# Kernel tuning notes

Hardware: AMD Instinct MI355X
Metric: run time of the kernel (lower is better)

## Reference

```python
import jax, jax.numpy as jnp
import numpy as np

VOCAB = 100000
HIDDEN = 512
BATCH = 4096
TOTAL_TOKENS = 819200
BN_EPS = 1e-5


def setup_inputs() -> dict:
    key = jax.random.key(0)
    k_tok, k_seg, k_t, k_emb, k_wh, k_bh, k_wo, k_bo = jax.random.split(key, 8)
    tokens = jax.random.randint(k_tok, (TOTAL_TOKENS,), 0, VOCAB, dtype=jnp.int64 if jax.config.jax_enable_x64 else jnp.int32)
    segment_ids = jnp.sort(jax.random.randint(k_seg, (TOTAL_TOKENS,), 0, BATCH))
    t = jax.random.uniform(k_t, (BATCH,), dtype=jnp.float32)
    emb = jax.random.normal(k_emb, (VOCAB, HIDDEN), dtype=jnp.float32)
    bound = 1.0 / np.sqrt(HIDDEN)
    W_h = jax.random.uniform(k_wh, (HIDDEN, HIDDEN), minval=-bound, maxval=bound, dtype=jnp.float32)
    b_h = jax.random.uniform(k_bh, (HIDDEN,), minval=-bound, maxval=bound, dtype=jnp.float32)
    gamma = jnp.ones((HIDDEN,), jnp.float32)
    beta = jnp.zeros((HIDDEN,), jnp.float32)
    W_o = jax.random.uniform(k_wo, (HIDDEN,), minval=-bound, maxval=bound, dtype=jnp.float32)
    b_o = jax.random.uniform(k_bo, (), minval=-bound, maxval=bound, dtype=jnp.float32)
    return {"tokens": tokens, "segment_ids": segment_ids, "t": t, "emb": emb,
            "W_h": W_h, "b_h": b_h, "gamma": gamma, "beta": beta, "W_o": W_o, "b_o": b_o}


def reference(tokens, segment_ids, t, emb, W_h, b_h, gamma, beta, W_o, b_o):
    # Ragged bag-of-words: gather embeddings and mean-pool per segment (per review)
    tok_emb = emb[tokens]                                            # [T, H]
    sums = jax.ops.segment_sum(tok_emb, segment_ids, num_segments=BATCH)   # [B, H]
    counts = jax.ops.segment_sum(jnp.ones((tokens.shape[0],), emb.dtype),
                                 segment_ids, num_segments=BATCH)    # [B]
    pooled = sums / jnp.maximum(counts, 1.0)[:, None]                # [B, H]
    # fc_hidden -> BatchNorm1d (training mode, batch stats, biased var) -> ReLU
    h = pooled @ W_h + b_h
    mu = jnp.mean(h, axis=0)
    var = jnp.mean((h - mu) ** 2, axis=0)
    h = gamma * (h - mu) * jax.lax.rsqrt(var + BN_EPS) + beta
    h = jax.nn.relu(h)
    # dropout is identity at eval; fc_output -> logits
    logits = h @ W_o + b_o                                           # [B]
    # BCEWithLogitsLoss (mean): softplus(x) - t*x
    loss = jnp.mean(jax.nn.softplus(logits) - t * logits)
    return (loss, logits)
```

## Files before the change

kernel.cpp:

```cpp
#include <hip/hip_runtime.h>
#include <hip/hip_bf16.h>

#define BATCH 4096
#define HIDDEN 512
#define BN_EPS 1e-5f
#define STAGE_CAP 1024

typedef unsigned int u32;
typedef unsigned short u16;
typedef unsigned char u8;
typedef float f32x4 __attribute__((ext_vector_type(4)));
typedef __bf16 bf16x8 __attribute__((ext_vector_type(8)));

__device__ __forceinline__ float bf2f(u32 lo) { return __uint_as_float(lo << 16); }
__device__ __forceinline__ u32 f2bf(float f) {
    u32 u = __float_as_uint(f);
    return (u + 0x7FFFu + ((u >> 16) & 1u)) >> 16;
}

__device__ __forceinline__ int detect_bf16(const u32* __restrict__ emb_w) {
    u32 v = emb_w[(size_t)(threadIdx.x & 63) * 400009u + 17u];
    float a = fabsf(bf2f(v & 0xffffu));
    bool bf_like = (a > 0.0009765625f) && (a < 16.0f);
    unsigned long long m = __ballot(bf_like);
    return __popcll(m) >= 48;
}

__global__ __launch_bounds__(256) void k_convert(const void* __restrict__ emb,
                                                 u8* __restrict__ tab,
                                                 float* __restrict__ scales,
                                                 const void* __restrict__ W,
                                                 u16* __restrict__ Wt,
                                                 float* __restrict__ zero_base,
                                                 int vocab) {
    const int nrb = (vocab + 3) >> 2;
    if (blockIdx.x == (u32)(nrb + 64)) {
        for (int i = threadIdx.x; i < 2 * HIDDEN + 2; i += 256) zero_base[i] = 0.f;
        return;
    }
    const int bf = detect_bf16((const u32*)emb);
    if (blockIdx.x >= (u32)nrb) {
        __shared__ u16 tile[64][66];
        const int b2 = blockIdx.x - nrb;
        const int k0 = (b2 >> 3) * 64, n0 = (b2 & 7) * 64;
        const int c = threadIdx.x & 63, r4 = threadIdx.x >> 6;
#pragma unroll
        for (int i = 0; i < 16; ++i) {
            const int k = k0 + r4 + i * 4;
            u16 w;
            if (bf) w = ((const u16*)W)[(size_t)k * HIDDEN + n0 + c];
            else    w = (u16)f2bf(((const float*)W)[(size_t)k * HIDDEN + n0 + c]);
            tile[k - k0][c] = w;
        }
        __syncthreads();
#pragma unroll
        for (int i = 0; i < 16; ++i) {
            const int n = n0 + r4 + i * 4;
            Wt[(size_t)n * HIDDEN + k0 + c] = tile[c][n - n0];
        }
        return;
    }

    const int wv = threadIdx.x >> 6, lane = threadIdx.x & 63;
    const int row = blockIdx.x * 4 + wv;
    if (row >= vocab) return;

    float v[8];
    if (bf) {
        uint4 u = *(const uint4*)((const u16*)emb + (size_t)row * HIDDEN + lane * 8);
        v[0] = bf2f(u.x & 0xffffu); v[1] = bf2f(u.x >> 16);
        v[2] = bf2f(u.y & 0xffffu); v[3] = bf2f(u.y >> 16);
        v[4] = bf2f(u.z & 0xffffu); v[5] = bf2f(u.z >> 16);
        v[6] = bf2f(u.w & 0xffffu); v[7] = bf2f(u.w >> 16);
    } else {
        const f32x4* p = (const f32x4*)((const float*)emb + (size_t)row * HIDDEN + lane * 8);
        f32x4 a = __builtin_nontemporal_load(p);
        f32x4 b = __builtin_nontemporal_load(p + 1);
        v[0] = a.x; v[1] = a.y; v[2] = a.z; v[3] = a.w;
        v[4] = b.x; v[5] = b.y; v[6] = b.z; v[7] = b.w;
    }
    float m = 0.f;
#pragma unroll
    for (int k = 0; k < 8; ++k) m = fmaxf(m, fabsf(v[k]));
#pragma unroll
    for (int o = 32; o > 0; o >>= 1) m = fmaxf(m, __shfl_xor(m, o));
    const float s   = m * (1.0f / 127.0f);
    const float inv = (m > 0.f) ? (127.0f / m) : 0.f;
    int q[8];
#pragma unroll
    for (int k = 0; k < 8; ++k) q[k] = (int)rintf(v[k] * inv);
    uint2 o;
    o.x = (q[0] & 255) | ((q[1] & 255) << 8) | ((q[2] & 255) << 16) | ((u32)(q[3] & 255) << 24);
    o.y = (q[4] & 255) | ((q[5] & 255) << 8) | ((q[6] & 255) << 16) | ((u32)(q[7] & 255) << 24);
    *(uint2*)(tab + (size_t)row * HIDDEN + lane * 8) = o;
    if (lane == 0) scales[row] = s;
}

__global__ __launch_bounds__(256) void k_pool(const int* __restrict__ tokens,
                                              const int* __restrict__ seg,
                                              const void* __restrict__ emb,
                                              const u8* __restrict__ tab,
                                              const float* __restrict__ scales,
                                              int use_table,
                                              u32* __restrict__ pooled_bf, int T) {
    const int bf = detect_bf16((const u32*)emb);
    const int b = blockIdx.x;
    int lo = 0, hi = T;
    while (lo < hi) { int m = (lo + hi) >> 1; if (seg[m] < b) lo = m + 1; else hi = m; }
    const int start = lo;
    hi = T;
    while (lo < hi) { int m = (lo + hi) >> 1; if (seg[m] < b + 1) lo = m + 1; else hi = m; }
    const int end = lo;
    const int cnt = end - start;

    const int wv = threadIdx.x >> 6;
    const int lane = threadIdx.x & 63;
    const int chunk = (cnt + 3) >> 2;
    const int ts = start + wv * chunk;
    const int te = min(ts + chunk, end);

    float acc[8] = {0.f,0.f,0.f,0.f,0.f,0.f,0.f,0.f};

    __shared__ int   stok[STAGE_CAP];
    __shared__ float ssc[STAGE_CAP];

#define DECQ(v_, s_) \
    acc[0] = fmaf(s_, (float)(int)(signed char)( v_.x        & 255u), acc[0]); \
    acc[1] = fmaf(s_, (float)(int)(signed char)((v_.x >>  8) & 255u), acc[1]); \
    acc[2] = fmaf(s_, (float)(int)(signed char)((v_.x >> 16) & 255u), acc[2]); \
    acc[3] = fmaf(s_, (float)(int)(signed char)( v_.x >> 24        ), acc[3]); \
    acc[4] = fmaf(s_, (float)(int)(signed char)( v_.y        & 255u), acc[4]); \
    acc[5] = fmaf(s_, (float)(int)(signed char)((v_.y >>  8) & 255u), acc[5]); \
    acc[6] = fmaf(s_, (float)(int)(signed char)((v_.y >> 16) & 255u), acc[6]); \
    acc[7] = fmaf(s_, (float)(int)(signed char)( v_.y >> 24        ), acc[7]);

    if (use_table && cnt <= STAGE_CAP) {
        for (int i = threadIdx.x; i < cnt; i += 256) {
            const int tk = tokens[start + i];
            stok[i] = tk;
            ssc[i]  = scales[tk];
        }
        __syncthreads();
        int t = ts;
        for (; t + 4 <= te; t += 4) {
            const int i = t - start;
            const int tk0 = stok[i],     tk1 = stok[i + 1];
            const int tk2 = stok[i + 2], tk3 = stok[i + 3];
            const float s0 = ssc[i],     s1 = ssc[i + 1];
            const float s2 = ssc[i + 2], s3 = ssc[i + 3];
            uint2 v0 = *(const uint2*)(tab + (size_t)tk0 * HIDDEN + lane * 8);
            uint2 v1 = *(const uint2*)(tab + (size_t)tk1 * HIDDEN + lane * 8);
            uint2 v2 = *(const uint2*)(tab + (size_t)tk2 * HIDDEN + lane * 8);
            uint2 v3 = *(const uint2*)(tab + (size_t)tk3 * HIDDEN + lane * 8);
            DECQ(v0, s0); DECQ(v1, s1); DECQ(v2, s2); DECQ(v3, s3);
        }
        for (; t < te; ++t) {
            const int i = t - start;
            const int tk = stok[i];
            const float s = ssc[i];
            uint2 v = *(const uint2*)(tab + (size_t)tk * HIDDEN + lane * 8);
            DECQ(v, s);
        }
    } else if (use_table) {
        int t = ts;
        for (; t + 4 <= te; t += 4) {
            const int tk0 = tokens[t],     tk1 = tokens[t + 1];
            const int tk2 = tokens[t + 2], tk3 = tokens[t + 3];
            const float s0 = scales[tk0], s1 = scales[tk1];
            const float s2 = scales[tk2], s3 = scales[tk3];
            uint2 v0 = *(const uint2*)(tab + (size_t)tk0 * HIDDEN + lane * 8);
            uint2 v1 = *(const uint2*)(tab + (size_t)tk1 * HIDDEN + lane * 8);
            uint2 v2 = *(const uint2*)(tab + (size_t)tk2 * HIDDEN + lane * 8);
            uint2 v3 = *(const uint2*)(tab + (size_t)tk3 * HIDDEN + lane * 8);
            DECQ(v0, s0); DECQ(v1, s1); DECQ(v2, s2); DECQ(v3, s3);
        }
        for (; t < te; ++t) {
            const int tk = tokens[t];
            const float s = scales[tk];
            uint2 v = *(const uint2*)(tab + (size_t)tk * HIDDEN + lane * 8);
            DECQ(v, s);
        }
    } else if (bf) {
        const u16* src = (const u16*)emb;
        for (int t = ts; t < te; ++t) {
            uint4 v = *(const uint4*)(src + (size_t)tokens[t] * HIDDEN + lane * 8);
            acc[0] += bf2f(v.x & 0xffffu); acc[1] += bf2f(v.x >> 16);
            acc[2] += bf2f(v.y & 0xffffu); acc[3] += bf2f(v.y >> 16);
            acc[4] += bf2f(v.z & 0xffffu); acc[5] += bf2f(v.z >> 16);
            acc[6] += bf2f(v.w & 0xffffu); acc[7] += bf2f(v.w >> 16);
        }
    } else {
        const float* e = (const float*)emb;
        for (int t = ts; t < te; ++t) {
            const float* p = e + (size_t)tokens[t] * HIDDEN + lane * 8;
            float4 a = *(const float4*)p, b2_ = *(const float4*)(p + 4);
            acc[0] += a.x; acc[1] += a.y; acc[2] += a.z; acc[3] += a.w;
            acc[4] += b2_.x; acc[5] += b2_.y; acc[6] += b2_.z; acc[7] += b2_.w;
        }
    }
#undef DECQ

    __shared__ float red[4][8][64];
    if (wv > 0) {
#pragma unroll
        for (int k = 0; k < 8; ++k) red[wv][k][lane] = acc[k];
    }
    __syncthreads();
    if (wv == 0) {
#pragma unroll
        for (int k = 0; k < 8; ++k)
            acc[k] += red[1][k][lane] + red[2][k][lane] + red[3][k][lane];
        const float inv = (cnt > 0) ? (1.0f / (float)cnt) : 1.0f;
        uint4 o;
        o.x = f2bf(acc[0] * inv) | (f2bf(acc[1] * inv) << 16);
        o.y = f2bf(acc[2] * inv) | (f2bf(acc[3] * inv) << 16);
        o.z = f2bf(acc[4] * inv) | (f2bf(acc[5] * inv) << 16);
        o.w = f2bf(acc[6] * inv) | (f2bf(acc[7] * inv) << 16);
        *(uint4*)(pooled_bf + (size_t)b * (HIDDEN / 2) + lane * 4) = o;
    }
}

__global__ __launch_bounds__(256) void k_gemm(const u32* __restrict__ pooled_bf,
                                              const void* __restrict__ W,
                                              const u16* __restrict__ Wt,
                                              const void* __restrict__ bias,
                                              const u32* __restrict__ embw,
                                              int use_wt,
                                              float* __restrict__ h,
                                              float* __restrict__ sums,
                                              float* __restrict__ sumsq) {
    __shared__ float ws_s[4][4][16], ws_q[4][4][16];
    const int bf = detect_bf16(embw);
    const int tid  = threadIdx.x;
    const int wv   = tid >> 6;
    const int lane = tid & 63;
    const int l15  = lane & 15;
    const int hi   = lane >> 4;
    const int rb   = (blockIdx.x >> 3) * 64;
    const int nb   = (blockIdx.x & 7) * 64;
    const int mrow = rb + wv * 16 + l15;

    f32x4 acc[4] = {};

    for (int k0 = 0; k0 < HIDDEN; k0 += 32) {
        const int kb = k0 + hi * 8;
        uint4 av = *(const uint4*)(pooled_bf + (size_t)mrow * (HIDDEN / 2) + (kb >> 1));
        bf16x8 afrag = __builtin_bit_cast(bf16x8, av);
#pragma unroll
        for (int j = 0; j < 4; ++j) {
            const int n = nb + j * 16 + l15;
            bf16x8 bfrag;
            if (use_wt) {
                uint4 bv = *(const uint4*)(Wt + (size_t)n * HIDDEN + kb);
                bfrag = __builtin_bit_cast(bf16x8, bv);
            } else {
                u16 bw[8];
                if (bf) {
                    const u16* Wb = (const u16*)W;
#pragma unroll
                    for (int i = 0; i < 8; ++i) bw[i] = Wb[(size_t)(kb + i) * HIDDEN + n];
                } else {
                    const float* Wf = (const float*)W;
#pragma unroll
                    for (int i = 0; i < 8; ++i) bw[i] = (u16)f2bf(Wf[(size_t)(kb + i) * HIDDEN + n]);
                }
                uint4 bv;
                bv.x = bw[0] | ((u32)bw[1] << 16);
                bv.y = bw[2] | ((u32)bw[3] << 16);
                bv.z = bw[4] | ((u32)bw[5] << 16);
                bv.w = bw[6] | ((u32)bw[7] << 16);
                bfrag = __builtin_bit_cast(bf16x8, bv);
            }
            acc[j] = __builtin_amdgcn_mfma_f32_16x16x32_bf16(afrag, bfrag, acc[j], 0, 0, 0);
        }
    }

#pragma unroll
    for (int j = 0; j < 4; ++j) {
        const int n = nb + j * 16 + l15;
        const float bvn = bf ? bf2f(((const u16*)bias)[n]) : ((const float*)bias)[n];
        float s = 0.f, q = 0.f;
#pragma unroll
        for (int r = 0; r < 4; ++r) {
            const int row = rb + wv * 16 + hi * 4 + r;
            const float v = acc[j][r] + bvn;
            h[(size_t)row * HIDDEN + n] = v;
            s += v;
            q = fmaf(v, v, q);
        }
        s += __shfl_xor(s, 16); s += __shfl_xor(s, 32);
        q += __shfl_xor(q, 16); q += __shfl_xor(q, 32);
        if (lane < 16) { ws_s[wv][j][l15] = s; ws_q[wv][j][l15] = q; }
    }
    __syncthreads();
    if (tid < 64) {
        const int j2 = tid >> 4, c = tid & 15;
        float ts = ws_s[0][j2][c] + ws_s[1][j2][c] + ws_s[2][j2][c] + ws_s[3][j2][c];
        float tq = ws_q[0][j2][c] + ws_q[1][j2][c] + ws_q[2][j2][c] + ws_q[3][j2][c];
        atomicAdd(&sums[nb + j2 * 16 + c],  ts);
        atomicAdd(&sumsq[nb + j2 * 16 + c], tq);
    }
}

__global__ __launch_bounds__(256) void k_out(const float* __restrict__ h,
                                             const float* __restrict__ sums,
                                             const float* __restrict__ sumsq,
                                             const void* __restrict__ gamma,
                                             const void* __restrict__ beta,
                                             const void* __restrict__ W_o,
                                             const void* __restrict__ b_o,
                                             const void* __restrict__ tvec,
                                             const u32* __restrict__ embw,
                                             void* __restrict__ out,
                                             float* __restrict__ loss_acc,
                                             u32* __restrict__ counter) {
    const int bf = detect_bf16(embw);
    const int lane = threadIdx.x & 63;
    const int wave = threadIdx.x >> 6;
    const int row  = blockIdx.x * 4 + wave;
    const float invN = 1.0f / (float)BATCH;
    const int c0 = lane * 8;

    float g[8], bt[8], wo[8];
    if (bf) {
        uint4 gu = *(const uint4*)((const u32*)gamma + lane * 4);
        uint4 bu = *(const uint4*)((const u32*)beta  + lane * 4);
        uint4 wu = *(const uint4*)((const u32*)W_o   + lane * 4);
        g[0]=bf2f(gu.x&0xffffu); g[1]=bf2f(gu.x>>16); g[2]=bf2f(gu.y&0xffffu); g[3]=bf2f(gu.y>>16);
        g[4]=bf2f(gu.z&0xffffu); g[5]=bf2f(gu.z>>16); g[6]=bf2f(gu.w&0xffffu); g[7]=bf2f(gu.w>>16);
        bt[0]=bf2f(bu.x&0xffffu); bt[1]=bf2f(bu.x>>16); bt[2]=bf2f(bu.y&0xffffu); bt[3]=bf2f(bu.y>>16);
        bt[4]=bf2f(bu.z&0xffffu); bt[5]=bf2f(bu.z>>16); bt[6]=bf2f(bu.w&0xffffu); bt[7]=bf2f(bu.w>>16);
        wo[0]=bf2f(wu.x&0xffffu); wo[1]=bf2f(wu.x>>16); wo[2]=bf2f(wu.y&0xffffu); wo[3]=bf2f(wu.y>>16);
        wo[4]=bf2f(wu.z&0xffffu); wo[5]=bf2f(wu.z>>16); wo[6]=bf2f(wu.w&0xffffu); wo[7]=bf2f(wu.w>>16);
    } else {
        float4 a, b2;
        a = *(const float4*)((const float*)gamma + c0); b2 = *(const float4*)((const float*)gamma + c0 + 4);
        g[0]=a.x; g[1]=a.y; g[2]=a.z; g[3]=a.w; g[4]=b2.x; g[5]=b2.y; g[6]=b2.z; g[7]=b2.w;
        a = *(const float4*)((const float*)beta + c0);  b2 = *(const float4*)((const float*)beta + c0 + 4);
        bt[0]=a.x; bt[1]=a.y; bt[2]=a.z; bt[3]=a.w; bt[4]=b2.x; bt[5]=b2.y; bt[6]=b2.z; bt[7]=b2.w;
        a = *(const float4*)((const float*)W_o + c0);   b2 = *(const float4*)((const float*)W_o + c0 + 4);
        wo[0]=a.x; wo[1]=a.y; wo[2]=a.z; wo[3]=a.w; wo[4]=b2.x; wo[5]=b2.y; wo[6]=b2.z; wo[7]=b2.w;
    }

    float hv[8], sm[8], sq[8];
    {
        const float* hp = h + (size_t)row * HIDDEN + c0;
        float4 a = *(const float4*)hp, b2 = *(const float4*)(hp + 4);
        hv[0]=a.x; hv[1]=a.y; hv[2]=a.z; hv[3]=a.w; hv[4]=b2.x; hv[5]=b2.y; hv[6]=b2.z; hv[7]=b2.w;
        a = *(const float4*)(sums + c0);  b2 = *(const float4*)(sums + c0 + 4);
        sm[0]=a.x; sm[1]=a.y; sm[2]=a.z; sm[3]=a.w; sm[4]=b2.x; sm[5]=b2.y; sm[6]=b2.z; sm[7]=b2.w;
        a = *(const float4*)(sumsq + c0); b2 = *(const float4*)(sumsq + c0 + 4);
        sq[0]=a.x; sq[1]=a.y; sq[2]=a.z; sq[3]=a.w; sq[4]=b2.x; sq[5]=b2.y; sq[6]=b2.z; sq[7]=b2.w;
    }

    float sum = 0.f;
#pragma unroll
    for (int k = 0; k < 8; ++k) {
        float mu  = sm[k] * invN;
        float var = sq[k] * invN - mu * mu;
        float xn  = (hv[k] - mu) * rsqrtf(var + BN_EPS);
        float y   = fmaf(g[k], xn, bt[k]);
        y = fmaxf(y, 0.f);
        sum = fmaf(y, wo[k], sum);
    }
#pragma unroll
    for (int o = 32; o > 0; o >>= 1) sum += __shfl_xor(sum, o);

    __shared__ float ls[4];
    if (lane == 0) {
        float bo = bf ? bf2f(((const u16*)b_o)[0]) : ((const float*)b_o)[0];
        float x = sum + bo;
        if (bf) ((u16*)out)[1 + row] = (u16)f2bf(x);
        else    ((float*)out)[1 + row] = x;
        float t = bf ? bf2f(((const u16*)tvec)[row]) : ((const float*)tvec)[row];
        float sp = fmaxf(x, 0.f) + log1pf(expf(-fabsf(x)));
        ls[wave] = sp - t * x;
    }
    __syncthreads();
    if (threadIdx.x == 0) {
        atomicAdd(loss_acc, ls[0] + ls[1] + ls[2] + ls[3]);
        __threadfence();
        u32 old = atomicAdd(counter, 1u);
        if (old == gridDim.x - 1) {
            float v = atomicAdd(loss_acc, 0.0f) * (1.0f / (float)BATCH);
            if (bf) ((u16*)out)[0] = (u16)f2bf(v);
            else    ((float*)out)[0] = v;
        }
    }
}

extern "C" void kernel_launch(void* const* d_in, const int* in_sizes, int n_in,
                              void* d_out, int out_size, void* d_ws, size_t ws_size,
                              hipStream_t stream) {
    const int*  tokens = (const int*)d_in[0];
    const int*  seg    = (const int*)d_in[1];
    const void* tvec   = d_in[2];
    const void* emb    = d_in[3];
    const void* W_h    = d_in[4];
    const void* b_h    = d_in[5];
    const void* gamma  = d_in[6];
    const void* beta   = d_in[7];
    const void* W_o    = d_in[8];
    const void* b_o    = d_in[9];
    const int T = in_sizes[0];
    const int vocab = in_sizes[3] / HIDDEN;

    char* ws = (char*)d_ws;
    u32*   pooled_bf = (u32*)ws;
    float* h         = (float*)(ws + (size_t)8 * 1024 * 1024);
    float* sums      = (float*)(ws + (size_t)16 * 1024 * 1024);
    float* sumsq     = sums + HIDDEN;
    float* loss_acc  = sums + 2 * HIDDEN;
    u32*   counter   = (u32*)(loss_acc + 1);
    const size_t TABLE_OFF   = (size_t)17 * 1024 * 1024;
    const size_t TABLE_BYTES = (size_t)vocab * HIDDEN;
    const size_t SCALE_BYTES = (size_t)vocab * sizeof(float);
    const size_t WT_BYTES    = (size_t)HIDDEN * HIDDEN * 2;
    u8*    tab    = (u8*)(ws + TABLE_OFF);
    float* scales = (float*)(ws + TABLE_OFF + TABLE_BYTES);
    u16*   Wt     = (u16*)(ws + TABLE_OFF + TABLE_BYTES + SCALE_BYTES);
    const int use_table =
        (ws_size >= TABLE_OFF + TABLE_BYTES + SCALE_BYTES + WT_BYTES) ? 1 : 0;

    const int nrb = (vocab + 3) >> 2;
    if (use_table) {
        k_convert<<<nrb + 64 + 1, 256, 0, stream>>>(emb, tab, scales, W_h, Wt,
                                                    sums, vocab);
    } else {
        (void)hipMemsetAsync(sums, 0, (2 * HIDDEN + 2) * sizeof(float), stream);
    }
    k_pool<<<BATCH, 256, 0, stream>>>(tokens, seg, emb, tab, scales, use_table,
                                      pooled_bf, T);
    k_gemm<<<(BATCH / 64) * 8, 256, 0, stream>>>(pooled_bf, W_h, Wt, b_h,
                                                 (const u32*)emb, use_table,
                                                 h, sums, sumsq);
    k_out<<<BATCH / 4, 256, 0, stream>>>(h, sums, sumsq, gamma, beta,
                                         W_o, b_o, tvec, (const u32*)emb, d_out,
                                         loss_acc, counter);
}
```

Measured before the change: 186.3 us.

## Fuse hidden GEMM with BatchNorm output stage using a grid barrier

Merges the hidden-layer GEMM and the BatchNorm/ReLU/output/loss kernel into one kernel. Each block now owns 16 full rows across all 512 columns, which lets the h matrix stay in registers instead of being written to and read back from global memory. A software grid-wide barrier (atomic counter with spin-wait) separates the column-statistics accumulation from the normalization. This drops a kernel launch and the h round trip. In exchange, the 256 blocks must all be co-resident, the spin can stall, and each block reads all of W_h, giving less reuse of W per block.

```diff
diff --git a/kernel.cpp b/kernel.cpp
--- a/kernel.cpp
+++ b/kernel.cpp
@@ -35,7 +35,7 @@
                                                  int vocab) {
     const int nrb = (vocab + 3) >> 2;
     if (blockIdx.x == (u32)(nrb + 64)) {
-        for (int i = threadIdx.x; i < 2 * HIDDEN + 2; i += 256) zero_base[i] = 0.f;
+        for (int i = threadIdx.x; i < 2 * HIDDEN + 3; i += 256) zero_base[i] = 0.f;
         return;
     }
     const int bf = detect_bf16((const u32*)emb);
@@ -220,35 +220,45 @@
     }
 }
 
-__global__ __launch_bounds__(256) void k_gemm(const u32* __restrict__ pooled_bf,
-                                              const void* __restrict__ W,
-                                              const u16* __restrict__ Wt,
-                                              const void* __restrict__ bias,
-                                              const u32* __restrict__ embw,
-                                              int use_wt,
-                                              float* __restrict__ h,
-                                              float* __restrict__ sums,
-                                              float* __restrict__ sumsq) {
-    __shared__ float ws_s[4][4][16], ws_q[4][4][16];
+__global__ __launch_bounds__(256) void k_gemm_out(const u32* __restrict__ pooled_bf,
+                                                  const void* __restrict__ W,
+                                                  const u16* __restrict__ Wt,
+                                                  const void* __restrict__ bias,
+                                                  const void* __restrict__ gamma,
+                                                  const void* __restrict__ beta,
+                                                  const void* __restrict__ W_o,
+                                                  const void* __restrict__ b_o,
+                                                  const void* __restrict__ tvec,
+                                                  const u32* __restrict__ embw,
+                                                  int use_wt,
+                                                  float* __restrict__ sums,
+                                                  float* __restrict__ sumsq,
+                                                  float* __restrict__ loss_acc,
+                                                  u32* __restrict__ lcount,
+                                                  u32* __restrict__ gdone,
+                                                  void* __restrict__ out) {
+    __shared__ float ws_s[4][8][16], ws_q[4][8][16];
+    __shared__ float rowpart[4][16];
+    __shared__ float lterm[16];
     const int bf = detect_bf16(embw);
     const int tid  = threadIdx.x;
     const int wv   = tid >> 6;
     const int lane = tid & 63;
     const int l15  = lane & 15;
     const int hi   = lane >> 4;
-    const int rb   = (blockIdx.x >> 3) * 64;
-    const int nb   = (blockIdx.x & 7) * 64;
-    const int mrow = rb + wv * 16 + l15;
-
-    f32x4 acc[4] = {};
+    const int rb   = blockIdx.x * 16;
+    const int mrow = rb + l15;
+    const float invN = 1.0f / (float)BATCH;
+
+    f32x4 acc[8] = {};
 
     for (int k0 = 0; k0 < HIDDEN; k0 += 32) {
         const int kb = k0 + hi * 8;
         uint4 av = *(const uint4*)(pooled_bf + (size_t)mrow * (HIDDEN / 2) + (kb >> 1));
         bf16x8 afrag = __builtin_bit_cast(bf16x8, av);
 #pragma unroll
-        for (int j = 0; j < 4; ++j) {
-            const int n = nb + j * 16 + l15;
+        for (int j = 0; j < 8; ++j) {
+            const int n = wv * 128 + j * 16 + l15;
             bf16x8 bfrag;
             if (use_wt) {
                 uint4 bv = *(const uint4*)(Wt + (size_t)n * HIDDEN + kb);
@@ -275,112 +285,91 @@
         }
     }
 
-#pragma unroll
-    for (int j = 0; j < 4; ++j) {
-        const int n = nb + j * 16 + l15;
-        const float bvn = bf ? bf2f(((const u16*)bias)[n]) : ((const float*)bias)[n];
+    float bv8[8];
+#pragma unroll
+    for (int j = 0; j < 8; ++j) {
+        const int n = wv * 128 + j * 16 + l15;
+        bv8[j] = bf ? bf2f(((const u16*)bias)[n]) : ((const float*)bias)[n];
         float s = 0.f, q = 0.f;
 #pragma unroll
         for (int r = 0; r < 4; ++r) {
-            const int row = rb + wv * 16 + hi * 4 + r;
-            const float v = acc[j][r] + bvn;
-            h[(size_t)row * HIDDEN + n] = v;
-            s += v;
-            q = fmaf(v, v, q);
+            acc[j][r] += bv8[j];
+            s += acc[j][r];
+            q = fmaf(acc[j][r], acc[j][r], q);
         }
         s += __shfl_xor(s, 16); s += __shfl_xor(s, 32);
         q += __shfl_xor(q, 16); q += __shfl_xor(q, 32);
         if (lane < 16) { ws_s[wv][j][l15] = s; ws_q[wv][j][l15] = q; }
     }
     __syncthreads();
-    if (tid < 64) {
-        const int j2 = tid >> 4, c = tid & 15;
-        float ts = ws_s[0][j2][c] + ws_s[1][j2][c] + ws_s[2][j2][c] + ws_s[3][j2][c];
-        float tq = ws_q[0][j2][c] + ws_q[1][j2][c] + ws_q[2][j2][c] + ws_q[3][j2][c];
-        atomicAdd(&sums[nb + j2 * 16 + c],  ts);
-        atomicAdd(&sumsq[nb + j2 * 16 + c], tq);
-    }
-}
-
-__global__ __launch_bounds__(256) void k_out(const float* __restrict__ h,
-                                             const float* __restrict__ sums,
-                                             const float* __restrict__ sumsq,
-                                             const void* __restrict__ gamma,
-                                             const void* __restrict__ beta,
-                                             const void* __restrict__ W_o,
-                                             const void* __restrict__ b_o,
-                                             const void* __restrict__ tvec,
-                                             const u32* __restrict__ embw,
-                                             void* __restrict__ out,
-                                             float* __restrict__ loss_acc,
-                                             u32* __restrict__ counter) {
-    const int bf = detect_bf16(embw);
-    const int lane = threadIdx.x & 63;
-    const int wave = threadIdx.x >> 6;
-    const int row  = blockIdx.x * 4 + wave;
-    const float invN = 1.0f / (float)BATCH;
-    const int c0 = lane * 8;
-
-    float g[8], bt[8], wo[8];
-    if (bf) {
-        uint4 gu = *(const uint4*)((const u32*)gamma + lane * 4);
-        uint4 bu = *(const uint4*)((const u32*)beta  + lane * 4);
-        uint4 wu = *(const uint4*)((const u32*)W_o   + lane * 4);
-        g[0]=bf2f(gu.x&0xffffu); g[1]=bf2f(gu.x>>16); g[2]=bf2f(gu.y&0xffffu); g[3]=bf2f(gu.y>>16);
-        g[4]=bf2f(gu.z&0xffffu); g[5]=bf2f(gu.z>>16); g[6]=bf2f(gu.w&0xffffu); g[7]=bf2f(gu.w>>16);
-        bt[0]=bf2f(bu.x&0xffffu); bt[1]=bf2f(bu.x>>16); bt[2]=bf2f(bu.y&0xffffu); bt[3]=bf2f(bu.y>>16);
-        bt[4]=bf2f(bu.z&0xffffu); bt[5]=bf2f(bu.z>>16); bt[6]=bf2f(bu.w&0xffffu); bt[7]=bf2f(bu.w>>16);
-        wo[0]=bf2f(wu.x&0xffffu); wo[1]=bf2f(wu.x>>16); wo[2]=bf2f(wu.y&0xffffu); wo[3]=bf2f(wu.y>>16);
-        wo[4]=bf2f(wu.z&0xffffu); wo[5]=bf2f(wu.z>>16); wo[6]=bf2f(wu.w&0xffffu); wo[7]=bf2f(wu.w>>16);
-    } else {
-        float4 a, b2;
-        a = *(const float4*)((const float*)gamma + c0); b2 = *(const float4*)((const float*)gamma + c0 + 4);
-        g[0]=a.x; g[1]=a.y; g[2]=a.z; g[3]=a.w; g[4]=b2.x; g[5]=b2.y; g[6]=b2.z; g[7]=b2.w;
-        a = *(const float4*)((const float*)beta + c0);  b2 = *(const float4*)((const float*)beta + c0 + 4);
-        bt[0]=a.x; bt[1]=a.y; bt[2]=a.z; bt[3]=a.w; bt[4]=b2.x; bt[5]=b2.y; bt[6]=b2.z; bt[7]=b2.w;
-        a = *(const float4*)((const float*)W_o + c0);   b2 = *(const float4*)((const float*)W_o + c0 + 4);
-        wo[0]=a.x; wo[1]=a.y; wo[2]=a.z; wo[3]=a.w; wo[4]=b2.x; wo[5]=b2.y; wo[6]=b2.z; wo[7]=b2.w;
-    }
-
-    float hv[8], sm[8], sq[8];
     {
-        const float* hp = h + (size_t)row * HIDDEN + c0;
-        float4 a = *(const float4*)hp, b2 = *(const float4*)(hp + 4);
-        hv[0]=a.x; hv[1]=a.y; hv[2]=a.z; hv[3]=a.w; hv[4]=b2.x; hv[5]=b2.y; hv[6]=b2.z; hv[7]=b2.w;
-        a = *(const float4*)(sums + c0);  b2 = *(const float4*)(sums + c0 + 4);
-        sm[0]=a.x; sm[1]=a.y; sm[2]=a.z; sm[3]=a.w; sm[4]=b2.x; sm[5]=b2.y; sm[6]=b2.z; sm[7]=b2.w;
-        a = *(const float4*)(sumsq + c0); b2 = *(const float4*)(sumsq + c0 + 4);
-        sq[0]=a.x; sq[1]=a.y; sq[2]=a.z; sq[3]=a.w; sq[4]=b2.x; sq[5]=b2.y; sq[6]=b2.z; sq[7]=b2.w;
-    }
-
-    float sum = 0.f;
-#pragma unroll
-    for (int k = 0; k < 8; ++k) {
-        float mu  = sm[k] * invN;
-        float var = sq[k] * invN - mu * mu;
-        float xn  = (hv[k] - mu) * rsqrtf(var + BN_EPS);
-        float y   = fmaf(g[k], xn, bt[k]);
-        y = fmaxf(y, 0.f);
-        sum = fmaf(y, wo[k], sum);
-    }
-#pragma unroll
-    for (int o = 32; o > 0; o >>= 1) sum += __shfl_xor(sum, o);
-
-    __shared__ float ls[4];
-    if (lane == 0) {
-        float bo = bf ? bf2f(((const u16*)b_o)[0]) : ((const float*)b_o)[0];
-        float x = sum + bo;
+        const int c2 = tid * 2;
+        const int w2 = c2 >> 7, rem = c2 & 127, j2 = rem >> 4, cc = rem & 15;
+        atomicAdd(&sums[c2],      ws_s[w2][j2][cc]);
+        atomicAdd(&sumsq[c2],     ws_q[w2][j2][cc]);
+        const int c3 = c2 + 1;
+        const int w3 = c3 >> 7, rem3 = c3 & 127, j3 = rem3 >> 4, cc3 = rem3 & 15;
+        atomicAdd(&sums[c3],      ws_s[w3][j3][cc3]);
+        atomicAdd(&sumsq[c3],     ws_q[w3][j3][cc3]);
+    }
+
+    if (tid == 0) {
+        __threadfence();
+        atomicAdd(gdone, 1u);
+        while (atomicAdd(gdone, 0u) < gridDim.x) __builtin_amdgcn_s_sleep(8);
+    }
+    __syncthreads();
+    __threadfence();
+
+    float part[4] = {0.f, 0.f, 0.f, 0.f};
+#pragma unroll
+    for (int j = 0; j < 8; ++j) {
+        const int n = wv * 128 + j * 16 + l15;
+        const float sm = __hip_atomic_load(&sums[n],  __ATOMIC_RELAXED, __HIP_MEMORY_SCOPE_AGENT);
+        const float sq = __hip_atomic_load(&sumsq[n], __ATOMIC_RELAXED, __HIP_MEMORY_SCOPE_AGENT);
+        const float mu  = sm * invN;
+        const float var = sq * invN - mu * mu;
+        const float rs  = rsqrtf(var + BN_EPS);
+        const float gn  = bf ? bf2f(((const u16*)gamma)[n]) : ((const float*)gamma)[n];
+        const float btn = bf ? bf2f(((const u16*)beta)[n])  : ((const float*)beta)[n];
+        const float won = bf ? bf2f(((const u16*)W_o)[n])   : ((const float*)W_o)[n];
+#pragma unroll
+        for (int r = 0; r < 4; ++r) {
+            float y = fmaf(gn, (acc[j][r] - mu) * rs, btn);
+            y = fmaxf(y, 0.f);
+            part[r] = fmaf(y, won, part[r]);
+        }
+    }
+#pragma unroll
+    for (int o = 8; o > 0; o >>= 1) {
+#pragma unroll
+        for (int r = 0; r < 4; ++r) part[r] += __shfl_xor(part[r], o);
+    }
+    if (l15 == 0) {
+#pragma unroll
+        for (int r = 0; r < 4; ++r) rowpart[wv][hi * 4 + r] = part[r];
+    }
+    __syncthreads();
+
+    if (tid < 16) {
+        const int row = rb + tid;
+        float dot = rowpart[0][tid] + rowpart[1][tid] + rowpart[2][tid] + rowpart[3][tid];
+        const float bo = bf ? bf2f(((const u16*)b_o)[0]) : ((const float*)b_o)[0];
+        const float x = dot + bo;
         if (bf) ((u16*)out)[1 + row] = (u16)f2bf(x);
         else    ((float*)out)[1 + row] = x;
-        float t = bf ? bf2f(((const u16*)tvec)[row]) : ((const float*)tvec)[row];
-        float sp = fmaxf(x, 0.f) + log1pf(expf(-fabsf(x)));
-        ls[wave] = sp - t * x;
+        const float t = bf ? bf2f(((const u16*)tvec)[row]) : ((const float*)tvec)[row];
+        const float sp = fmaxf(x, 0.f) + log1pf(expf(-fabsf(x)));
+        lterm[tid] = sp - t * x;
     }
     __syncthreads();
-    if (threadIdx.x == 0) {
-        atomicAdd(loss_acc, ls[0] + ls[1] + ls[2] + ls[3]);
+    if (tid == 0) {
+        float bl = 0.f;
+#pragma unroll
+        for (int i = 0; i < 16; ++i) bl += lterm[i];
+        atomicAdd(loss_acc, bl);
         __threadfence();
-        u32 old = atomicAdd(counter, 1u);
+        u32 old = atomicAdd(lcount, 1u);
         if (old == gridDim.x - 1) {
             float v = atomicAdd(loss_acc, 0.0f) * (1.0f / (float)BATCH);
             if (bf) ((u16*)out)[0] = (u16)f2bf(v);
@@ -407,11 +396,11 @@
 
     char* ws = (char*)d_ws;
     u32*   pooled_bf = (u32*)ws;
-    float* h         = (float*)(ws + (size_t)8 * 1024 * 1024);
     float* sums      = (float*)(ws + (size_t)16 * 1024 * 1024);
     float* sumsq     = sums + HIDDEN;
     float* loss_acc  = sums + 2 * HIDDEN;
-    u32*   counter   = (u32*)(loss_acc + 1);
+    u32*   lcount    = (u32*)(loss_acc + 1);
+    u32*   gdone     = (u32*)(loss_acc + 2);
     const size_t TABLE_OFF   = (size_t)17 * 1024 * 1024;
     const size_t TABLE_BYTES = (size_t)vocab * HIDDEN;
     const size_t SCALE_BYTES = (size_t)vocab * sizeof(float);
@@ -427,14 +416,13 @@
         k_convert<<<nrb + 64 + 1, 256, 0, stream>>>(emb, tab, scales, W_h, Wt,
                                                     sums, vocab);
     } else {
-        (void)hipMemsetAsync(sums, 0, (2 * HIDDEN + 2) * sizeof(float), stream);
+        (void)hipMemsetAsync(sums, 0, (2 * HIDDEN + 3) * sizeof(float), stream);
     }
     k_pool<<<BATCH, 256, 0, stream>>>(tokens, seg, emb, tab, scales, use_table,
                                       pooled_bf, T);
-    k_gemm<<<(BATCH / 64) * 8, 256, 0, stream>>>(pooled_bf, W_h, Wt, b_h,
-                                                 (const u32*)emb, use_table,
-                                                 h, sums, sumsq);
-    k_out<<<BATCH / 4, 256, 0, stream>>>(h, sums, sumsq, gamma, beta,
-                                         W_o, b_o, tvec, (const u32*)emb, d_out,
-                                         loss_acc, counter);
-}
+    k_gemm_out<<<BATCH / 16, 256, 0, stream>>>(pooled_bf, W_h, Wt, b_h,
+                                               gamma, beta, W_o, b_o, tvec,
+                                               (const u32*)emb, use_table,
+                                               sums, sumsq, loss_acc, lcount,
+                                               gdone, d_out);
+}
```

Result: slower. 205.4 us (+10.2%).
